# Kernel tuning notes

Measured on AMD Instinct MI355X. Metric: run time of the kernel, lower is better.

Reference implementation:

```python
import jax, jax.numpy as jnp
import numpy as np

N_NODES = 20000
N_EDGES = 320000
D = 256          # out_channels (== in_channels here, so PyG zero-padding is a no-op)
NUM_LAYERS = 5


def setup_inputs() -> dict:
    key = jax.random.key(0)
    ks = jax.random.split(key, 8)
    x = jax.random.normal(ks[0], (N_NODES, D), dtype=jnp.float32)
    src = jax.random.randint(ks[1], (N_EDGES,), 0, N_NODES)
    dst = jax.random.randint(ks[2], (N_EDGES,), 0, N_NODES)
    edge_index = jnp.stack([src, dst]).astype(jnp.int64)
    edge_attr = jax.random.uniform(ks[3], (N_EDGES,), dtype=jnp.float32)
    s = 1.0 / np.sqrt(D)
    # per-layer message transform weights [L, D, D]
    weight = jax.random.uniform(ks[4], (NUM_LAYERS, D, D), minval=-s, maxval=s, dtype=jnp.float32)
    # GRUCell parameters (torch layout: [3*D, D] for W_ih/W_hh, [3*D] biases; gate order r, z, n)
    w_ih = jax.random.uniform(ks[5], (3 * D, D), minval=-s, maxval=s, dtype=jnp.float32)
    w_hh = jax.random.uniform(ks[6], (3 * D, D), minval=-s, maxval=s, dtype=jnp.float32)
    b = jax.random.uniform(ks[7], (2, 3 * D), minval=-s, maxval=s, dtype=jnp.float32)
    return {"x": x, "edge_index": edge_index, "edge_attr": edge_attr,
            "weight": weight, "w_ih": w_ih, "w_hh": w_hh,
            "b_ih": b[0], "b_hh": b[1]}


def gru_cell(m, h, w_ih, w_hh, b_ih, b_hh):
    gi = m @ w_ih.T + b_ih   # [N, 3D]
    gh = h @ w_hh.T + b_hh   # [N, 3D]
    i_r, i_z, i_n = jnp.split(gi, 3, axis=1)
    h_r, h_z, h_n = jnp.split(gh, 3, axis=1)
    r = jax.nn.sigmoid(i_r + h_r)
    z = jax.nn.sigmoid(i_z + h_z)
    n = jnp.tanh(i_n + r * h_n)
    return (1.0 - z) * n + z * h


def reference(x, edge_index, edge_attr, weight, w_ih, w_hh, b_ih, b_hh):
    src = edge_index[0]
    dst = edge_index[1]
    n_nodes = x.shape[0]
    h = x  # in_channels == out_channels, so no zero padding needed
    for i in range(weight.shape[0]):
        m = h @ weight[i]                                  # [N, D] transformed messages
        msgs = m[src] * edge_attr[:, None]                 # gather + edge weighting [E, D]
        agg = jax.ops.segment_sum(msgs, dst, num_segments=n_nodes)  # scatter-add [N, D]
        h = gru_cell(agg, h, w_ih, w_hh, b_ih, b_hh)
    return h
```

## Files before the change

### kernel.cpp

```cpp
#include <hip/hip_runtime.h>
#include <hip/hip_bf16.h>

#define NN 20000
#define NE 320000
#define DD 256

typedef __attribute__((ext_vector_type(8))) short bf16x8;
typedef __attribute__((ext_vector_type(4))) float f32x4;
typedef __attribute__((ext_vector_type(4))) int   int4v;
typedef __attribute__((ext_vector_type(4))) float float4v;

typedef __attribute__((address_space(1))) unsigned int gas_uint;
typedef __attribute__((address_space(3))) unsigned int las_uint;
static __device__ __forceinline__ void gload16(const void* g, void* l) {
    __builtin_amdgcn_global_load_lds((gas_uint*)g, (las_uint*)l, 16, 0, 0);
}

__device__ __forceinline__ unsigned short f2bf(float f) {
    union { float f; unsigned u; } v; v.f = f;
    unsigned r = v.u + 0x7fffu + ((v.u >> 16) & 1u);
    return (unsigned short)(r >> 16);
}
__device__ __forceinline__ float bf2f(unsigned short h) {
    union { unsigned u; float f; } v; v.u = ((unsigned)h) << 16;
    return v.f;
}
__device__ __forceinline__ float fast_sigmoid(float x) {
    return 1.f / (1.f + __expf(-x));
}
__device__ __forceinline__ float fast_tanh(float x) {
    x = fminf(fmaxf(x, -30.f), 30.f);
    float e = __expf(-2.f * x);
    return (1.f - e) / (1.f + e);
}


__global__ void cast_kernel(const float* __restrict__ in, unsigned short* __restrict__ out, int n) {
    int i = (blockIdx.x * blockDim.x + threadIdx.x) * 4;
    if (i >= n) return;
    float4v v = *reinterpret_cast<const float4v*>(in + i);
    uint2 o;
    o.x = (unsigned)f2bf(v.x) | ((unsigned)f2bf(v.y) << 16);
    o.y = (unsigned)f2bf(v.z) | ((unsigned)f2bf(v.w) << 16);
    *reinterpret_cast<uint2*>(out + i) = o;
}

__global__ __launch_bounds__(256) void pgemm_kernel(const unsigned short* __restrict__ A,
                                                    const unsigned short* __restrict__ Bt,
                                                    unsigned short* __restrict__ C) {
    __shared__ __align__(16) unsigned short As[128 * 64];
    __shared__ __align__(16) unsigned short Bs[64 * 64];
    const int t = threadIdx.x;
    const int lane = t & 63;
    const int w = t >> 6;
    const int wr = w >> 1, wc = w & 1;
    const int m0 = blockIdx.y * 128;
    const int n0 = blockIdx.x * 64;

    f32x4 acc[4][2];
    const f32x4 z4 = {0.f, 0.f, 0.f, 0.f};
    for (int i = 0; i < 4; ++i) for (int j = 0; j < 2; ++j) acc[i][j] = z4;

    for (int kt = 0; kt < 4; ++kt) {
        const int k0 = kt * 64;
#pragma unroll
        for (int rnd = 0; rnd < 4; ++rnd) {
            int cb = rnd * 256 + (w << 6);
            int c = cb + lane;
            int row = c >> 3, sl = c & 7;
            int gsl = sl ^ (row & 7);
            gload16(A + (size_t)(m0 + row) * 256 + k0 + gsl * 8, &As[cb * 8]);
        }
#pragma unroll
        for (int rnd = 0; rnd < 2; ++rnd) {
            int cb = rnd * 256 + (w << 6);
            int c = cb + lane;
            int row = c >> 3, sl = c & 7;
            int gsl = sl ^ (row & 7);
            gload16(Bt + (size_t)(n0 + row) * 256 + k0 + gsl * 8, &Bs[cb * 8]);
        }
        __syncthreads();
#pragma unroll
        for (int ks = 0; ks < 2; ++ks) {
            const int slot = ks * 4 + (lane >> 4);
            bf16x8 a[4], b[2];
#pragma unroll
            for (int mi = 0; mi < 4; ++mi) {
                int row = wr * 64 + mi * 16 + (lane & 15);
                a[mi] = *reinterpret_cast<const bf16x8*>(&As[row * 64 + ((slot ^ (row & 7)) << 3)]);
            }
#pragma unroll
            for (int ni = 0; ni < 2; ++ni) {
                int row = wc * 32 + ni * 16 + (lane & 15);
                b[ni] = *reinterpret_cast<const bf16x8*>(&Bs[row * 64 + ((slot ^ (row & 7)) << 3)]);
            }
#pragma unroll
            for (int mi = 0; mi < 4; ++mi)
#pragma unroll
                for (int ni = 0; ni < 2; ++ni)
                    acc[mi][ni] = __builtin_amdgcn_mfma_f32_16x16x32_bf16(a[mi], b[ni], acc[mi][ni], 0, 0, 0);
        }
        __syncthreads();
    }
#pragma unroll
    for (int mi = 0; mi < 4; ++mi)
#pragma unroll
        for (int ni = 0; ni < 2; ++ni)
#pragma unroll
            for (int r = 0; r < 4; ++r) {
                int grow = m0 + wr * 64 + mi * 16 + (lane >> 4) * 4 + r;
                int gcol = n0 + wc * 32 + ni * 16 + (lane & 15);
                C[(size_t)grow * 768 + gcol] = f2bf(acc[mi][ni][r]);
            }
}

__global__ void wc5_kernel(const unsigned short* __restrict__ Pall,
                           const float* __restrict__ whh,
                           unsigned short* __restrict__ Wc5) {
    int id = blockIdx.x * 256 + threadIdx.x;
    int k  = id & 255;
    int t2 = id >> 8;
    int n3 = t2 % 768;
    int t3 = t2 / 768;
    int hf = t3 & 1;
    int l  = t3 >> 1;
    int g3 = (n3 >> 4) % 3;
    int dg = n3 / 48;
    int dc = n3 & 15;
    int d  = dg * 16 + dc;
    int gate_row = g3 * 256 + d;
    unsigned short v;
    if (hf == 0) v = Pall[((size_t)(l * 256 + k)) * 768 + gate_row];
    else         v = f2bf(whh[(size_t)gate_row * 256 + k]);
    Wc5[id] = v;
}


__global__ void hist_kernel(const int* __restrict__ dst, int* __restrict__ deg) {
    int e = blockIdx.x * 256 + threadIdx.x;
    if (e < NE) atomicAdd(&deg[dst[e]], 1);
}

__global__ __launch_bounds__(1024) void scan_kernel(const int* __restrict__ deg, int* __restrict__ base) {
    __shared__ int part[1024];
    const int t = threadIdx.x;
    const int CH = 20;
    int start = t * CH;
    int s = 0;
    for (int i = 0; i < CH; ++i) { int idx = start + i; if (idx < NN) s += deg[idx]; }
    part[t] = s; __syncthreads();
    for (int off = 1; off < 1024; off <<= 1) {
        int v = (t >= off) ? part[t - off] : 0;
        __syncthreads();
        part[t] += v;
        __syncthreads();
    }
    int run = (t == 0) ? 0 : part[t - 1];
    for (int i = 0; i < CH; ++i) {
        int idx = start + i;
        if (idx < NN) { base[idx] = run; run += deg[idx]; }
    }
    if (t == 1023) base[NN] = run;
}

__global__ void fill_kernel(const int* __restrict__ src, const int* __restrict__ dst,
                            const float* __restrict__ attr, const int* __restrict__ base,
                            int* __restrict__ cursor, int* __restrict__ ssrc,
                            float* __restrict__ sattr) {
    int e = blockIdx.x * 256 + threadIdx.x;
    if (e >= NE) return;
    int d = dst[e];
    int pos = base[d] + atomicAdd(&cursor[d], 1);
    ssrc[pos] = src[e];
    sattr[pos] = attr[e];
}

__global__ __launch_bounds__(256) void gather_agg_kernel(const unsigned short* __restrict__ Hbf,
                                                         const int* __restrict__ base,
                                                         const int* __restrict__ ssrc,
                                                         const float* __restrict__ sattr,
                                                         unsigned short* __restrict__ AggBf) {
    int node = blockIdx.x * 4 + (threadIdx.x >> 6);
    if (node >= NN) return;
    int lane = threadIdx.x & 63;
    int half = lane >> 5;
    int dl = lane & 31;
    int b0 = base[node], b1 = base[node + 1];
    float ac[8] = {0.f, 0.f, 0.f, 0.f, 0.f, 0.f, 0.f, 0.f};
    for (int p = b0 + half; p < b1; p += 2) {
        int s = ssrc[p];
        float a = sattr[p];
        int4v v = *reinterpret_cast<const int4v*>(Hbf + (size_t)s * 256 + dl * 8);
        ac[0] += a * bf2f((unsigned short)(v.x & 0xffff));
        ac[1] += a * bf2f((unsigned short)((unsigned)v.x >> 16));
        ac[2] += a * bf2f((unsigned short)(v.y & 0xffff));
        ac[3] += a * bf2f((unsigned short)((unsigned)v.y >> 16));
        ac[4] += a * bf2f((unsigned short)(v.z & 0xffff));
        ac[5] += a * bf2f((unsigned short)((unsigned)v.z >> 16));
        ac[6] += a * bf2f((unsigned short)(v.w & 0xffff));
        ac[7] += a * bf2f((unsigned short)((unsigned)v.w >> 16));
    }
#pragma unroll
    for (int j = 0; j < 8; ++j) ac[j] += __shfl_xor(ac[j], 32);
    if (half == 0) {
        int4v o;
        o.x = (int)((unsigned)f2bf(ac[0]) | ((unsigned)f2bf(ac[1]) << 16));
        o.y = (int)((unsigned)f2bf(ac[2]) | ((unsigned)f2bf(ac[3]) << 16));
        o.z = (int)((unsigned)f2bf(ac[4]) | ((unsigned)f2bf(ac[5]) << 16));
        o.w = (int)((unsigned)f2bf(ac[6]) | ((unsigned)f2bf(ac[7]) << 16));
        *reinterpret_cast<int4v*>(AggBf + (size_t)node * 256 + dl * 8) = o;
    }
}

__global__ __launch_bounds__(256) void gru2_kernel(const unsigned short* __restrict__ Abf,
                                                   const unsigned short* __restrict__ Hbf,
                                                   const unsigned short* __restrict__ Wc,
                                                   const float* __restrict__ b_ih,
                                                   const float* __restrict__ b_hh,
                                                   const float* __restrict__ x_f32,
                                                   float* __restrict__ h_out,
                                                   unsigned short* __restrict__ Hbf_out,
                                                   int first, int last) {
    __shared__ __align__(16) unsigned short As[128 * 64];
    __shared__ __align__(16) unsigned short Bs[48 * 64];
    const int t = threadIdx.x;
    const int lane = t & 63;
    const int w = t >> 6;
    int b = blockIdx.x;
    int ww = (b & 7) * 316 + (b >> 3);
    const int mt = ww >> 4, dg = ww & 15;
    const int m0 = mt * 128;

    f32x4 aR[2], aZ[2], aI[2], aH[2];
    const f32x4 z4 = {0.f, 0.f, 0.f, 0.f};
#pragma unroll
    for (int i = 0; i < 2; ++i) { aR[i] = z4; aZ[i] = z4; aI[i] = z4; aH[i] = z4; }

    auto do_half = [&](const unsigned short* __restrict__ aptr,
                       const unsigned short* __restrict__ wcb,
                       f32x4 (&aX)[2]) {
        for (int kq = 0; kq < 4; ++kq) {
            const int ka = kq * 64;
#pragma unroll
            for (int rnd = 0; rnd < 4; ++rnd) {
                int cb = rnd * 256 + (w << 6);
                int c = cb + lane;
                int row = c >> 3, sl = c & 7;
                int gsl = sl ^ (row & 7);
                gload16(aptr + (size_t)(m0 + row) * 256 + ka + gsl * 8, &As[cb * 8]);
            }
            {
                int cb = (w << 6);
                int c = cb + lane;
                int row = c >> 3, sl = c & 7;
                int gsl = sl ^ (row & 7);
                gload16(wcb + (size_t)(dg * 48 + row) * 256 + ka + gsl * 8, &Bs[cb * 8]);
            }
            if (w < 2) {
                int cb = 256 + (w << 6);
                int c = cb + lane;
                int row = c >> 3, sl = c & 7;
                int gsl = sl ^ (row & 7);
                gload16(wcb + (size_t)(dg * 48 + row) * 256 + ka + gsl * 8, &Bs[cb * 8]);
            }
            __syncthreads();
#pragma unroll
            for (int ks = 0; ks < 2; ++ks) {
                const int slot = ks * 4 + (lane >> 4);
                bf16x8 a[2], bfr[3];
#pragma unroll
                for (int mi = 0; mi < 2; ++mi) {
                    int row = w * 32 + mi * 16 + (lane & 15);
                    a[mi] = *reinterpret_cast<const bf16x8*>(&As[row * 64 + ((slot ^ (row & 7)) << 3)]);
                }
#pragma unroll
                for (int g3 = 0; g3 < 3; ++g3) {
                    int row = g3 * 16 + (lane & 15);
                    bfr[g3] = *reinterpret_cast<const bf16x8*>(&Bs[row * 64 + ((slot ^ (row & 7)) << 3)]);
                }
#pragma unroll
                for (int mi = 0; mi < 2; ++mi) {
                    aR[mi] = __builtin_amdgcn_mfma_f32_16x16x32_bf16(a[mi], bfr[0], aR[mi], 0, 0, 0);
                    aZ[mi] = __builtin_amdgcn_mfma_f32_16x16x32_bf16(a[mi], bfr[1], aZ[mi], 0, 0, 0);
                    aX[mi] = __builtin_amdgcn_mfma_f32_16x16x32_bf16(a[mi], bfr[2], aX[mi], 0, 0, 0);
                }
            }
            __syncthreads();
        }
    };

    do_half(Abf, Wc, aI);
    do_half(Hbf, Wc + 768 * 256, aH);

    const int d = dg * 16 + (lane & 15);
    const float bir = b_ih[d],        bhr = b_hh[d];
    const float biz = b_ih[256 + d],  bhz = b_hh[256 + d];
    const float bin_ = b_ih[512 + d], bhn = b_hh[512 + d];
#pragma unroll
    for (int mi = 0; mi < 2; ++mi)
#pragma unroll
        for (int r = 0; r < 4; ++r) {
            int grow = m0 + w * 32 + mi * 16 + (lane >> 4) * 4 + r;
            if (grow >= NN) continue;
            size_t idx = (size_t)grow * 256 + d;
            float rr = fast_sigmoid(aR[mi][r] + bir + bhr);
            float zz = fast_sigmoid(aZ[mi][r] + biz + bhz);
            float nn = fast_tanh(aI[mi][r] + bin_ + rr * (aH[mi][r] + bhn));
            float hp = first ? x_f32[idx] : bf2f(Hbf[idx]);
            float hv = (1.f - zz) * nn + zz * hp;
            if (last) h_out[idx] = hv;
            Hbf_out[idx] = f2bf(hv);
        }
}


extern "C" void kernel_launch(void* const* d_in, const int* in_sizes, int n_in,
                              void* d_out, int out_size, void* d_ws, size_t ws_size,
                              hipStream_t stream) {
    const float* x     = (const float*)d_in[0];
    const int*   eidx  = (const int*)d_in[1];
    const float* eattr = (const float*)d_in[2];
    const float* W     = (const float*)d_in[3];
    const float* wih   = (const float*)d_in[4];
    const float* whh   = (const float*)d_in[5];
    const float* bih   = (const float*)d_in[6];
    const float* bhh   = (const float*)d_in[7];
    float* out = (float*)d_out;
    const int* esrc = eidx;
    const int* edst = eidx + NE;

    char* p = (char*)d_ws;
    auto alloc = [&](size_t bytes) -> char* {
        char* r = p; p += (bytes + 255) & ~(size_t)255; return r;
    };
    unsigned short* hbfA  = (unsigned short*)alloc((size_t)NN * DD * 2);
    unsigned short* hbfB  = (unsigned short*)alloc((size_t)NN * DD * 2);
    unsigned short* aggbf = (unsigned short*)alloc((size_t)NN * DD * 2);
    unsigned short* wnb   = (unsigned short*)alloc((size_t)5 * DD * DD * 2);
    unsigned short* wihb  = (unsigned short*)alloc((size_t)768 * DD * 2);
    unsigned short* pall  = (unsigned short*)alloc((size_t)1280 * 768 * 2);
    unsigned short* wc5   = (unsigned short*)alloc((size_t)5 * 2 * 768 * 256 * 2);
    int*   deg    = (int*)alloc((size_t)NN * 4);
    int*   basep  = (int*)alloc((size_t)(NN + 1) * 4);
    int*   cursor = (int*)alloc((size_t)NN * 4);
    int*   ssrc   = (int*)alloc((size_t)NE * 4);
    float* sattr  = (float*)alloc((size_t)NE * 4);
    alloc(262144);

    hipMemsetAsync(deg, 0, (size_t)NN * 4, stream);
    hipMemsetAsync(cursor, 0, (size_t)NN * 4, stream);

    cast_kernel<<<320, 256, 0, stream>>>(W, wnb, 5 * DD * DD);
    cast_kernel<<<192, 256, 0, stream>>>(wih, wihb, 768 * DD);
    cast_kernel<<<5000, 256, 0, stream>>>(x, hbfA, NN * DD);
    pgemm_kernel<<<dim3(12, 10), 256, 0, stream>>>(wnb, wihb, pall);
    wc5_kernel<<<7680, 256, 0, stream>>>(pall, whh, wc5);
    hist_kernel<<<1250, 256, 0, stream>>>(edst, deg);
    scan_kernel<<<1, 1024, 0, stream>>>(deg, basep);
    fill_kernel<<<1250, 256, 0, stream>>>(esrc, edst, eattr, basep, cursor, ssrc, sattr);

    unsigned short* hb_cur = hbfA;
    unsigned short* hb_nxt = hbfB;
    for (int l = 0; l < 5; ++l) {
        gather_agg_kernel<<<5000, 256, 0, stream>>>(hb_cur, basep, ssrc, sattr, aggbf);
        gru2_kernel<<<2528, 256, 0, stream>>>(aggbf, hb_cur, wc5 + (size_t)l * 2 * 768 * 256,
                                              bih, bhh, x, out, hb_nxt,
                                              (l == 0) ? 1 : 0, (l == 4) ? 1 : 0);
        unsigned short* tmp = hb_cur; hb_cur = hb_nxt; hb_nxt = tmp;
    }
    (void)in_sizes; (void)n_in; (void)out_size; (void)ws_size;
}
```

Baseline: 383.4 us.

## Widen GRU GEMM row tile to 256 and split gather across four edge lanes

New measurement: 409.4 us. 1.07x slower.

```diff
diff --git a/kernel.cpp b/kernel.cpp
--- a/kernel.cpp
+++ b/kernel.cpp
@@ -183,36 +183,45 @@
     int node = blockIdx.x * 4 + (threadIdx.x >> 6);
     if (node >= NN) return;
     int lane = threadIdx.x & 63;
-    int half = lane >> 5;
-    int dl = lane & 31;
+    int q = lane >> 4;
+    int ql = lane & 15;
     int b0 = base[node], b1 = base[node + 1];
-    float ac[8] = {0.f, 0.f, 0.f, 0.f, 0.f, 0.f, 0.f, 0.f};
-    for (int p = b0 + half; p < b1; p += 2) {
+    float ac[16];
+#pragma unroll
+    for (int j = 0; j < 16; ++j) ac[j] = 0.f;
+    for (int p = b0 + q; p < b1; p += 4) {
         int s = ssrc[p];
         float a = sattr[p];
-        int4v v = *reinterpret_cast<const int4v*>(Hbf + (size_t)s * 256 + dl * 8);
-        ac[0] += a * bf2f((unsigned short)(v.x & 0xffff));
-        ac[1] += a * bf2f((unsigned short)((unsigned)v.x >> 16));
-        ac[2] += a * bf2f((unsigned short)(v.y & 0xffff));
-        ac[3] += a * bf2f((unsigned short)((unsigned)v.y >> 16));
-        ac[4] += a * bf2f((unsigned short)(v.z & 0xffff));
-        ac[5] += a * bf2f((unsigned short)((unsigned)v.z >> 16));
-        ac[6] += a * bf2f((unsigned short)(v.w & 0xffff));
-        ac[7] += a * bf2f((unsigned short)((unsigned)v.w >> 16));
-    }
-#pragma unroll
-    for (int j = 0; j < 8; ++j) ac[j] += __shfl_xor(ac[j], 32);
-    if (half == 0) {
-        int4v o;
-        o.x = (int)((unsigned)f2bf(ac[0]) | ((unsigned)f2bf(ac[1]) << 16));
-        o.y = (int)((unsigned)f2bf(ac[2]) | ((unsigned)f2bf(ac[3]) << 16));
-        o.z = (int)((unsigned)f2bf(ac[4]) | ((unsigned)f2bf(ac[5]) << 16));
-        o.w = (int)((unsigned)f2bf(ac[6]) | ((unsigned)f2bf(ac[7]) << 16));
-        *reinterpret_cast<int4v*>(AggBf + (size_t)node * 256 + dl * 8) = o;
-    }
-}
-
-__global__ __launch_bounds__(256) void gru2_kernel(const unsigned short* __restrict__ Abf,
+        const unsigned short* rowp = Hbf + (size_t)s * 256 + ql * 16;
+        int4v v0 = *reinterpret_cast<const int4v*>(rowp);
+        int4v v1 = *reinterpret_cast<const int4v*>(rowp + 8);
+#pragma unroll
+        for (int j = 0; j < 4; ++j) {
+            unsigned u0 = (unsigned)v0[j];
+            ac[2 * j]     += a * bf2f((unsigned short)(u0 & 0xffff));
+            ac[2 * j + 1] += a * bf2f((unsigned short)(u0 >> 16));
+            unsigned u1 = (unsigned)v1[j];
+            ac[8 + 2 * j]     += a * bf2f((unsigned short)(u1 & 0xffff));
+            ac[8 + 2 * j + 1] += a * bf2f((unsigned short)(u1 >> 16));
+        }
+    }
+#pragma unroll
+    for (int j = 0; j < 16; ++j) {
+        ac[j] += __shfl_xor(ac[j], 16);
+        ac[j] += __shfl_xor(ac[j], 32);
+    }
+    if (q == 0) {
+        unsigned ou[8];
+#pragma unroll
+        for (int j = 0; j < 8; ++j)
+            ou[j] = (unsigned)f2bf(ac[2 * j]) | ((unsigned)f2bf(ac[2 * j + 1]) << 16);
+        unsigned short* op = AggBf + (size_t)node * 256 + ql * 16;
+        *reinterpret_cast<int4v*>(op)     = *reinterpret_cast<int4v*>(&ou[0]);
+        *reinterpret_cast<int4v*>(op + 8) = *reinterpret_cast<int4v*>(&ou[4]);
+    }
+}
+
+__global__ __launch_bounds__(256) void gru3_kernel(const unsigned short* __restrict__ Abf,
                                                    const unsigned short* __restrict__ Hbf,
                                                    const unsigned short* __restrict__ Wc,
                                                    const float* __restrict__ b_ih,
@@ -221,28 +230,28 @@
                                                    float* __restrict__ h_out,
                                                    unsigned short* __restrict__ Hbf_out,
                                                    int first, int last) {
-    __shared__ __align__(16) unsigned short As[128 * 64];
+    __shared__ __align__(16) unsigned short As[256 * 64];
     __shared__ __align__(16) unsigned short Bs[48 * 64];
     const int t = threadIdx.x;
     const int lane = t & 63;
     const int w = t >> 6;
     int b = blockIdx.x;
-    int ww = (b & 7) * 316 + (b >> 3);
+    int ww = (b & 7) * 158 + (b >> 3);
     const int mt = ww >> 4, dg = ww & 15;
-    const int m0 = mt * 128;
-
-    f32x4 aR[2], aZ[2], aI[2], aH[2];
+    const int m0 = mt * 256;
+
+    f32x4 aR[4], aZ[4], aI[4], aH[4];
     const f32x4 z4 = {0.f, 0.f, 0.f, 0.f};
 #pragma unroll
-    for (int i = 0; i < 2; ++i) { aR[i] = z4; aZ[i] = z4; aI[i] = z4; aH[i] = z4; }
+    for (int i = 0; i < 4; ++i) { aR[i] = z4; aZ[i] = z4; aI[i] = z4; aH[i] = z4; }
 
     auto do_half = [&](const unsigned short* __restrict__ aptr,
                        const unsigned short* __restrict__ wcb,
-                       f32x4 (&aX)[2]) {
+                       f32x4 (&aX)[4]) {
         for (int kq = 0; kq < 4; ++kq) {
             const int ka = kq * 64;
 #pragma unroll
-            for (int rnd = 0; rnd < 4; ++rnd) {
+            for (int rnd = 0; rnd < 8; ++rnd) {
                 int cb = rnd * 256 + (w << 6);
                 int c = cb + lane;
                 int row = c >> 3, sl = c & 7;
@@ -267,10 +276,10 @@
 #pragma unroll
             for (int ks = 0; ks < 2; ++ks) {
                 const int slot = ks * 4 + (lane >> 4);
-                bf16x8 a[2], bfr[3];
-#pragma unroll
-                for (int mi = 0; mi < 2; ++mi) {
-                    int row = w * 32 + mi * 16 + (lane & 15);
+                bf16x8 a[4], bfr[3];
+#pragma unroll
+                for (int mi = 0; mi < 4; ++mi) {
+                    int row = w * 64 + mi * 16 + (lane & 15);
                     a[mi] = *reinterpret_cast<const bf16x8*>(&As[row * 64 + ((slot ^ (row & 7)) << 3)]);
                 }
 #pragma unroll
@@ -279,7 +288,7 @@
                     bfr[g3] = *reinterpret_cast<const bf16x8*>(&Bs[row * 64 + ((slot ^ (row & 7)) << 3)]);
                 }
 #pragma unroll
-                for (int mi = 0; mi < 2; ++mi) {
+                for (int mi = 0; mi < 4; ++mi) {
                     aR[mi] = __builtin_amdgcn_mfma_f32_16x16x32_bf16(a[mi], bfr[0], aR[mi], 0, 0, 0);
                     aZ[mi] = __builtin_amdgcn_mfma_f32_16x16x32_bf16(a[mi], bfr[1], aZ[mi], 0, 0, 0);
                     aX[mi] = __builtin_amdgcn_mfma_f32_16x16x32_bf16(a[mi], bfr[2], aX[mi], 0, 0, 0);
@@ -297,10 +306,10 @@
     const float biz = b_ih[256 + d],  bhz = b_hh[256 + d];
     const float bin_ = b_ih[512 + d], bhn = b_hh[512 + d];
 #pragma unroll
-    for (int mi = 0; mi < 2; ++mi)
+    for (int mi = 0; mi < 4; ++mi)
 #pragma unroll
         for (int r = 0; r < 4; ++r) {
-            int grow = m0 + w * 32 + mi * 16 + (lane >> 4) * 4 + r;
+            int grow = m0 + w * 64 + mi * 16 + (lane >> 4) * 4 + r;
             if (grow >= NN) continue;
             size_t idx = (size_t)grow * 256 + d;
             float rr = fast_sigmoid(aR[mi][r] + bir + bhr);
@@ -363,7 +372,7 @@
     unsigned short* hb_nxt = hbfB;
     for (int l = 0; l < 5; ++l) {
         gather_agg_kernel<<<5000, 256, 0, stream>>>(hb_cur, basep, ssrc, sattr, aggbf);
-        gru2_kernel<<<2528, 256, 0, stream>>>(aggbf, hb_cur, wc5 + (size_t)l * 2 * 768 * 256,
+        gru3_kernel<<<1264, 256, 0, stream>>>(aggbf, hb_cur, wc5 + (size_t)l * 2 * 768 * 256,
                                               bih, bhh, x, out, hb_nxt,
                                               (l == 0) ? 1 : 0, (l == 4) ? 1 : 0);
         unsigned short* tmp = hb_cur; hb_cur = hb_nxt; hb_nxt = tmp;
```
